# Performance work log

Measured on AMD Instinct MI355X. Metric: run time of the kernel, lower is better.

The kernel has to match this reference:

```python
import jax, jax.numpy as jnp
import numpy as np

B, T, DF, S = 64, 16, 512, 196      # batch, ticks, backbone channels, tokens
D_IN, H = 512, 8                     # attention embed dim, heads
DH = D_IN // H
DM, MEM, HN = 1024, 25, 32           # d_model neurons, memory length, NLM hidden
NSA, NSO, DOUT = 512, 512, 512       # sync sizes (random-pairing), output dim


def _ln(x, g, b, eps=1e-5):
    m = x.mean(-1, keepdims=True)
    v = ((x - m) ** 2).mean(-1, keepdims=True)
    return (x - m) / jnp.sqrt(v + eps) * g + b


def setup_inputs() -> dict:
    key = jax.random.key(0)
    ks = jax.random.split(key, 24)
    rn = lambda k, sh, sc: jax.random.normal(k, sh, jnp.float32) * sc
    p = {}
    p['x'] = rn(ks[0], (B, T, DF, S), 1.0)
    # q_proj (LazyLinear: n_sync_action -> d_input)
    p['Wqp'] = rn(ks[1], (NSA, D_IN), (1.0 / NSA) ** 0.5); p['bqp'] = jnp.zeros((D_IN,))
    # kv_proj: LazyLinear(DF->D_IN) + LayerNorm
    p['Wkv'] = rn(ks[2], (DF, D_IN), (1.0 / DF) ** 0.5); p['bkv'] = jnp.zeros((D_IN,))
    p['g_kv'] = jnp.ones((D_IN,)); p['b_kv'] = jnp.zeros((D_IN,))
    # MultiheadAttention projections
    sc = (1.0 / D_IN) ** 0.5
    p['Wq'] = rn(ks[3], (D_IN, D_IN), sc); p['bq'] = jnp.zeros((D_IN,))
    p['Wk'] = rn(ks[4], (D_IN, D_IN), sc); p['bk'] = jnp.zeros((D_IN,))
    p['Wv'] = rn(ks[5], (D_IN, D_IN), sc); p['bv'] = jnp.zeros((D_IN,))
    p['Wo'] = rn(ks[6], (D_IN, D_IN), sc); p['bo'] = jnp.zeros((D_IN,))
    # synapses: Linear(D_IN+DM -> 2*DM) + GLU + LayerNorm(DM)
    p['Wsyn'] = rn(ks[7], (D_IN + DM, 2 * DM), (1.0 / (D_IN + DM)) ** 0.5)
    p['bsyn'] = jnp.zeros((2 * DM,))
    p['g_syn'] = jnp.ones((DM,)); p['b_syn'] = jnp.zeros((DM,))
    # NLM: per-neuron 2-layer MLP over memory window
    p['W1'] = rn(ks[8], (DM, MEM, HN), (1.0 / MEM) ** 0.5); p['b1'] = jnp.zeros((DM, HN))
    p['W2'] = rn(ks[9], (DM, HN), (1.0 / HN) ** 0.5); p['b2'] = jnp.zeros((DM,))
    # learned initial states
    p['init_act'] = rn(ks[10], (DM,), (1.0 / DM) ** 0.5)
    p['init_hist'] = rn(ks[11], (DM, MEM), (1.0 / (DM + MEM)) ** 0.5)
    # decay params (init zero in torch)
    p['decay_a'] = jnp.zeros((NSA,)); p['decay_o'] = jnp.zeros((NSO,))
    # output projection (LazyLinear: n_sync_out -> d_output)
    p['Wout'] = rn(ks[12], (NSO, DOUT), (1.0 / NSO) ** 0.5); p['bout'] = jnp.zeros((DOUT,))
    # random-pairing neuron indices (buffers, constants)
    p['li_a'] = jax.random.randint(ks[13], (NSA,), 0, DM, jnp.int32)
    p['ri_a'] = jax.random.randint(ks[14], (NSA,), 0, DM, jnp.int32)
    p['li_o'] = jax.random.randint(ks[15], (NSO,), 0, DM, jnp.int32)
    p['ri_o'] = jax.random.randint(ks[16], (NSO,), 0, DM, jnp.int32)
    return p


def reference(x, Wqp, bqp, Wkv, bkv, g_kv, b_kv, Wq, bq, Wk, bk, Wv, bv, Wo, bo,
              Wsyn, bsyn, g_syn, b_syn, W1, b1, W2, b2, init_act, init_hist,
              decay_a, decay_o, Wout, bout, li_a, ri_a, li_o, ri_o):
    r_a = jnp.exp(-jnp.clip(decay_a, 0.0, 15.0))   # [NSA]
    r_o = jnp.exp(-jnp.clip(decay_o, 0.0, 15.0))   # [NSO]
    act0 = jnp.broadcast_to(init_act, (B, DM))
    hist0 = jnp.broadcast_to(init_hist, (B, DM, MEM))
    # initial 'out' sync state (decay_alpha=pairwise, decay_beta=ones)
    ao0 = act0[:, li_o] * act0[:, ri_o]
    bo0 = jnp.ones_like(ao0)
    # 'action' state starts None -> zeros so first update gives alpha=pairwise, beta=1
    aa0 = jnp.zeros((B, NSA), x.dtype); ba0 = jnp.zeros((B, NSA), x.dtype)

    def mha(q, kv):
        # q [B,1,D_IN], kv [B,S,D_IN]
        qh = (q @ Wq + bq).reshape(B, 1, H, DH)
        kh = (kv @ Wk + bk).reshape(B, S, H, DH)
        vh = (kv @ Wv + bv).reshape(B, S, H, DH)
        sc = jnp.einsum('bqhd,bkhd->bhqk', qh, kh) / jnp.sqrt(jnp.float32(DH))
        a = jax.nn.softmax(sc, axis=-1)
        o = jnp.einsum('bhqk,bkhd->bqhd', a, vh).reshape(B, 1, D_IN)
        return o @ Wo + bo

    def tick(carry, xt):
        act, hist, aa, ba, ao, bo_ = carry
        # compute_kv: identity backbone, flatten(2).transpose(1,2) -> [B,S,DF]
        kv = _ln(jnp.swapaxes(xt, 1, 2) @ Wkv + bkv, g_kv, b_kv)
        # action sync
        aa = r_a * aa + act[:, li_a] * act[:, ri_a]
        ba = r_a * ba + 1.0
        sync_a = aa / jnp.sqrt(ba)
        q = (sync_a @ Wqp + bqp)[:, None, :]
        attn = mha(q, kv)[:, 0]                         # [B,D_IN]
        pre = jnp.concatenate([attn, act], axis=-1)     # [B,D_IN+DM]
        g = pre @ Wsyn + bsyn
        a_, b_ = jnp.split(g, 2, axis=-1)
        pre_act = _ln(a_ * jax.nn.sigmoid(b_), g_syn, b_syn)  # [B,DM]
        hist = jnp.concatenate([hist[:, :, 1:], pre_act[:, :, None]], axis=2)
        # NLM: per-neuron MLP over memory window
        h = jax.nn.relu(jnp.einsum('bnm,nmh->bnh', hist, W1) + b1)
        act = jnp.einsum('bnh,nh->bn', h, W2) + b2
        # out sync
        ao = r_o * ao + act[:, li_o] * act[:, ri_o]
        bo_ = r_o * bo_ + 1.0
        sync_o = ao / jnp.sqrt(bo_)
        pred = sync_o @ Wout + bout                      # [B,DOUT]
        logp = jax.nn.log_softmax(pred, axis=-1)
        ne = -(jnp.exp(logp) * logp).sum(-1) / jnp.log(jnp.float32(DOUT))
        cert = jnp.stack([ne, 1.0 - ne], axis=-1)        # [B,2]
        return (act, hist, aa, ba, ao, bo_), (pred, cert)

    xt = jnp.moveaxis(x, 1, 0)  # [T,B,DF,S]
    _, (preds, certs) = jax.lax.scan(tick, (act0, hist0, aa0, ba0, ao0, bo0), xt)
    predictions = jnp.moveaxis(preds, 0, -1)   # [B,DOUT,T]
    certainties = jnp.moveaxis(certs, 0, -1)   # [B,2,T]
    return predictions, certainties
```

## Files before the change

kernel.cpp:

```cpp
#include <hip/hip_runtime.h>
#include <stdint.h>
#include <stddef.h>

#define B_    64
#define T_    16
#define DF_   512
#define S_    196
#define DIN_  512
#define H_    8
#define DH_   64
#define DM_   1024
#define MEM_  25
#define HN_   32
#define MR_   (B_*S_)
#define TC_   2
#define NCH_  (T_/TC_)
#define MCC_  (MR_*TC_)

typedef short bf16x8 __attribute__((ext_vector_type(8)));
typedef short short4v __attribute__((ext_vector_type(4)));
typedef float f32x4  __attribute__((ext_vector_type(4)));

__device__ __forceinline__ float b2f(short h){
  unsigned u = ((unsigned)(unsigned short)h) << 16;
  float f; __builtin_memcpy(&f, &u, 4); return f;
}
__device__ __forceinline__ short f2b(float f){
  unsigned u; __builtin_memcpy(&u, &f, 4);
  u = (u + 0x7fffu + ((u >> 16) & 1u)) >> 16;
  return (short)(unsigned short)u;
}
__device__ __forceinline__ float clip015(float d){
  return d < 0.f ? 0.f : (d > 15.f ? 15.f : d);
}

template<int OUTF32, int LNEPI>
__device__ __forceinline__ void gemm_body(int tid, int bx, int by, int aload,
    short* lA, short* lB,
    const short* __restrict__ A, const short* __restrict__ WT,
    void* __restrict__ Cout,
    const float* __restrict__ biasA, const float* __restrict__ biasB, int nsplit,
    const float* __restrict__ mu, const float* __restrict__ iv,
    const float* __restrict__ gw, const float* __restrict__ bw,
    int M, int N, int K, int lda, int ldc)
{
  const int w = tid >> 6, l = tid & 63;
  const int m0 = bx * 128, n0 = by * 128;
  const int wm = (w >> 1) * 64, wn = (w & 1) * 64;
  f32x4 acc[4][4];
  #pragma unroll
  for (int i=0;i<4;i++)
    #pragma unroll
    for (int j=0;j<4;j++) acc[i][j] = (f32x4){0.f,0.f,0.f,0.f};

  for (int k0 = 0; k0 < K; k0 += 64) {
    #pragma unroll
    for (int rnd = 0; rnd < 4; ++rnd) {
      int cb = (rnd*4 + w) * 64;
      int slot = cb + l;
      int row = slot >> 3, kb = slot & 7;
      int kc = k0 + ((kb ^ (row & 7)) << 3);
      if (aload) {
        int gm = m0 + row; if (gm > M-1) gm = M-1;
        __builtin_amdgcn_global_load_lds(
            (const __attribute__((address_space(1))) void*)(A + (size_t)gm * lda + kc),
            (__attribute__((address_space(3))) void*)&lA[cb*8], 16, 0, 0);
      }
      __builtin_amdgcn_global_load_lds(
          (const __attribute__((address_space(1))) void*)(WT + (size_t)(n0 + row) * K + kc),
          (__attribute__((address_space(3))) void*)&lB[cb*8], 16, 0, 0);
    }
    asm volatile("s_waitcnt vmcnt(0)" ::: "memory");
    __syncthreads();
    #pragma unroll
    for (int ks = 0; ks < 2; ++ks) {
      bf16x8 af[4], bfr[4];
      #pragma unroll
      for (int i = 0; i < 4; ++i) {
        int ra = wm + i*16 + (l & 15);
        int c  = ks*4 + (l >> 4);
        af[i]  = *(const bf16x8*)&lA[ra*64 + ((c ^ (ra & 7)) << 3)];
        int rb = wn + i*16 + (l & 15);
        bfr[i] = *(const bf16x8*)&lB[rb*64 + ((c ^ (rb & 7)) << 3)];
      }
      #pragma unroll
      for (int i = 0; i < 4; ++i)
        #pragma unroll
        for (int j = 0; j < 4; ++j)
          acc[i][j] = __builtin_amdgcn_mfma_f32_16x16x32_bf16(af[i], bfr[j], acc[i][j], 0, 0, 0);
    }
    __syncthreads();
  }
  #pragma unroll
  for (int i = 0; i < 4; ++i) {
    #pragma unroll
    for (int j = 0; j < 4; ++j) {
      int gn = n0 + wn + j*16 + (l & 15);
      float ivn = 0.f, mun = 0.f, bb = 0.f;
      if (LNEPI == 2) { ivn = iv[gn]; mun = mu[gn]; }
      else bb = biasA ? ((gn < nsplit) ? biasA[gn] : biasB[gn - nsplit]) : 0.f;
      #pragma unroll
      for (int r = 0; r < 4; ++r) {
        int gm = m0 + wm + i*16 + (l >> 4)*4 + r;
        if (gm < M) {
          float v;
          if (LNEPI == 2) v = ivn*(acc[i][j][r] - mun*gw[gm]) + bw[gm];
          else            v = acc[i][j][r] + bb;
          if (OUTF32) ((float*)Cout)[(size_t)gm * ldc + gn] = v;
          else        ((short*)Cout)[(size_t)gm * ldc + gn] = f2b(v);
        }
      }
    }
  }
}

template<int OUTF32, int LNEPI>
__global__ __launch_bounds__(256,2) void gemm_k(
    const short* __restrict__ A, const short* __restrict__ WT,
    void* __restrict__ Cout,
    const float* __restrict__ biasA, const float* __restrict__ biasB, int nsplit,
    const float* __restrict__ mu, const float* __restrict__ iv,
    const float* __restrict__ gw, const float* __restrict__ bw,
    int M, int N, int K, int lda, int ldc)
{
  __shared__ short lA[128*64];
  __shared__ short lB[128*64];
  gemm_body<OUTF32,LNEPI>(threadIdx.x, blockIdx.x, blockIdx.y, 1, lA, lB,
                          A, WT, Cout, biasA, biasB, nsplit, mu, iv, gw, bw,
                          M, N, K, lda, ldc);
}

__global__ __launch_bounds__(256,2) void gemm_prep2(
    const short* __restrict__ WqpB, const short* __restrict__ WqT,
    short* __restrict__ WqqB,
    const short* __restrict__ WsynTt, const short* __restrict__ WoB,
    short* __restrict__ WsynF)
{
  __shared__ short lA[128*64];
  __shared__ short lB[128*64];
  int blk = blockIdx.x;
  if (blk < 16)
    gemm_body<0,0>(threadIdx.x, blk & 3, blk >> 2, 1, lA, lB, WqpB, WqT, WqqB,
                   nullptr, nullptr, 1<<30, nullptr, nullptr, nullptr, nullptr,
                   512, 512, 512, 512, 512);
  else {
    int b2 = blk - 16;
    gemm_body<0,0>(threadIdx.x, b2 & 15, b2 >> 4, 1, lA, lB, WsynTt, WoB, WsynF,
                   nullptr, nullptr, 1<<30, nullptr, nullptr, nullptr, nullptr,
                   2048, 512, 512, 512, 1536);
  }
}

__device__ __forceinline__ void run_piggy(int tid, int pb, int pop, int poff,
    char* pool,
    const float* __restrict__ xg, int t0n, short* __restrict__ xT,
    const short* __restrict__ WkvT, const float* __restrict__ bkv,
    short* __restrict__ kvpN, float* __restrict__ muN, float* __restrict__ ivN,
    const short* __restrict__ WkkvT, const float* __restrict__ gw,
    const float* __restrict__ bw, short* __restrict__ KVTN, int McN)
{
  if (pop == 4) {
    int twin = tid >> 8, tid2 = tid & 255;
    float* tile = (float*)(pool + twin*8448);
    int tx = tid2 & 31, ty = tid2 >> 5;
    int base = (poff + pb)*32 + twin*16;
    for (int it = 0; it < 16; ++it) {
      int gt = base + it;
      int df0 = (gt & 15) * 32;
      int r = gt >> 4;
      int s0 = (r % 7) * 32;
      int z = r / 7;
      int b = z >> 1, ti = z & 1;
      const float* src = xg + (size_t)(b*T_ + t0n + ti) * DF_ * S_;
      #pragma unroll
      for (int i = 0; i < 4; ++i) {
        int df = df0 + ty + i*8;
        int s  = s0 + tx;
        tile[(ty+i*8)*33 + tx] = (s < S_) ? src[(size_t)df*S_ + s] : 0.f;
      }
      __syncthreads();
      short* dst = xT + (size_t)((t0n + ti)*B_ + b) * S_ * DIN_;
      #pragma unroll
      for (int i = 0; i < 4; ++i) {
        int s  = s0 + ty + i*8;
        int df = df0 + tx;
        if (s < S_) dst[(size_t)s*DF_ + df] = f2b(tile[tx*33 + ty+i*8]);
      }
      __syncthreads();
    }
  } else if (pop == 1) {
    int twin = tid >> 8;
    short* lA = (short*)pool;
    short* lB = (short*)(pool + 16384 + 16384*twin);
    int p = poff + pb; if (p > 391) p = 391;
    int bx = p % 196, byp = p / 196;
    const short* xTn = xT + (size_t)t0n * MR_ * 512;
    gemm_body<0,0>(tid & 255, bx, byp*2 + twin, twin == 0, lA, lB,
                   xTn, WkvT, kvpN, bkv, bkv, 1 << 30,
                   nullptr, nullptr, nullptr, nullptr,
                   McN, 512, 512, 512, 512);
  } else if (pop == 2) {
    int blk = poff + pb;
    int w = tid >> 6, l = tid & 63;
    for (int i = 0; i < 8; ++i) {
      int r = blk*64 + i*8 + w;
      if (r < McN) {
        bf16x8 v8 = *(const bf16x8*)&kvpN[(size_t)r*512 + l*8];
        float s = 0.f, s2 = 0.f;
        #pragma unroll
        for (int j = 0; j < 8; ++j) { float v = b2f(v8[j]); s += v; s2 += v*v; }
        #pragma unroll
        for (int m = 1; m < 64; m <<= 1) { s += __shfl_xor(s, m, 64); s2 += __shfl_xor(s2, m, 64); }
        if (l == 0) {
          float mean = s * (1.f/512.f);
          float var  = s2 * (1.f/512.f) - mean*mean;
          muN[r] = mean;
          ivN[r] = rsqrtf(var + 1e-5f);
        }
      }
    }
  } else if (pop == 3) {
    int twin = tid >> 8;
    short* lA = (short*)pool;
    short* lB = (short*)(pool + 16384 + 16384*twin);
    int p = poff + pb; if (p > 783) p = 783;
    int bx = p % 8, byp = p / 8;
    gemm_body<0,2>(tid & 255, bx, byp*2 + twin, twin == 0, lA, lB,
                   WkkvT, kvpN, KVTN, nullptr, nullptr, 0,
                   muN, ivN, gw, bw, 1024, McN, 512, 512, McN);
  }
}

__device__ __forceinline__ void attn_body(int b, int tid, float* smem,
    const float* actT, float* aa, float* ba,
    const int* li_a, const int* ri_a, const float* decay_a,
    const short* WqqB, const float* bqh,
    const short* KVT, int ldkv, int ti, short* preb)
{
  float* syncL = smem;
  float* qhL   = smem + 512;
  float* pL    = smem + 1024;
  int j = tid;
  float rr = expf(-clip015(decay_a[j]));
  float prod = actT[li_a[j]*64 + b] * actT[ri_a[j]*64 + b];
  float a2 = rr*aa[b*512+j] + prod; aa[b*512+j] = a2;
  float bb2 = rr*ba[b*512+j] + 1.f;  ba[b*512+j] = bb2;
  syncL[j] = a2 * rsqrtf(bb2);
  __syncthreads();
  float qa = bqh[j];
  #pragma unroll 8
  for (int k = 0; k < 512; ++k) qa += syncL[k]*b2f(WqqB[k*512+j]);
  qhL[j] = qa;
  __syncthreads();
  int h = tid >> 6, l = tid & 63;
  const size_t cb = (size_t)(ti*B_ + b) * S_;
  const short* Kb = KVT + (size_t)(h*64)*ldkv + cb;
  int s3 = 192 + l; int s3c = s3 < S_ ? s3 : S_-1;
  float sc0=0.f, sc1=0.f, sc2=0.f, sc3=0.f;
  #pragma unroll 8
  for (int d = 0; d < 64; ++d) {
    const short* kr = Kb + (size_t)d*ldkv;
    float qv = qhL[h*64 + d];
    sc0 += qv * b2f(kr[l]);
    sc1 += qv * b2f(kr[64 + l]);
    sc2 += qv * b2f(kr[128 + l]);
    sc3 += qv * b2f(kr[s3c]);
  }
  sc0 *= 0.125f; sc1 *= 0.125f; sc2 *= 0.125f;
  sc3 = (s3 < S_) ? sc3*0.125f : -1e30f;
  float mx = fmaxf(fmaxf(sc0, sc1), fmaxf(sc2, sc3));
  #pragma unroll
  for (int k = 32; k >= 1; k >>= 1) mx = fmaxf(mx, __shfl_xor(mx, k, 64));
  float p0 = expf(sc0-mx), p1 = expf(sc1-mx), p2 = expf(sc2-mx), p3 = expf(sc3-mx);
  pL[h*256 + l] = p0; pL[h*256 + 64+l] = p1;
  pL[h*256 + 128+l] = p2; pL[h*256 + 192+l] = p3;
  float ps = p0+p1+p2+p3;
  #pragma unroll
  for (int k = 32; k >= 1; k >>= 1) ps += __shfl_xor(ps, k, 64);
  float inv = 1.f / ps;
  __syncthreads();
  const short4v* vrow = (const short4v*)(KVT + (size_t)(512 + h*64 + l)*ldkv + cb);
  const float* pp = pL + h*256;
  float ac0=0.f, ac1=0.f, ac2=0.f, ac3=0.f;
  #pragma unroll 7
  for (int c = 0; c < 49; ++c) {
    short4v v4 = vrow[c];
    ac0 += pp[c*4]   * b2f(v4.x);
    ac1 += pp[c*4+1] * b2f(v4.y);
    ac2 += pp[c*4+2] * b2f(v4.z);
    ac3 += pp[c*4+3] * b2f(v4.w);
  }
  float accv = (ac0+ac1)+(ac2+ac3);
  preb[(size_t)b*1536 + h*64 + l] = f2b(accv * inv);
}

__device__ __forceinline__ void outk_body(int tt, int b, int tid,
    float* syncL, float* wred,
    const float* actT, float* ao, float* bo_s,
    const int* li_o, const int* ri_o, const float* decay_o,
    const short* WoutB, const float* bout, float* out)
{
  int j = tid;
  float rr = expf(-clip015(decay_o[j]));
  float prod = actT[li_o[j]*64 + b] * actT[ri_o[j]*64 + b];
  float a2 = rr*ao[b*512+j] + prod; ao[b*512+j] = a2;
  float bb2 = rr*bo_s[b*512+j] + 1.f; bo_s[b*512+j] = bb2;
  syncL[j] = a2 * rsqrtf(bb2);
  __syncthreads();
  float a = bout[j];
  #pragma unroll 8
  for (int k = 0; k < 512; ++k) a += syncL[k]*b2f(WoutB[k*512+j]);
  out[((size_t)b*512 + j)*16 + tt] = a;
  int w = tid >> 6, l = tid & 63;
  float m = a;
  #pragma unroll
  for (int k = 32; k >= 1; k >>= 1) m = fmaxf(m, __shfl_xor(m, k, 64));
  if (l == 0) wred[w] = m;
  __syncthreads();
  float M = wred[0];
  #pragma unroll
  for (int k = 1; k < 8; ++k) M = fmaxf(M, wred[k]);
  float e = expf(a - M);
  float z = e, s1 = e*(a - M);
  #pragma unroll
  for (int k = 32; k >= 1; k >>= 1) { z += __shfl_xor(z, k, 64); s1 += __shfl_xor(s1, k, 64); }
  if (l == 0) { wred[8+w] = z; wred[16+w] = s1; }
  __syncthreads();
  if (tid == 0) {
    float Z = 0.f, S1 = 0.f;
    #pragma unroll
    for (int k = 0; k < 8; ++k) { Z += wred[8+k]; S1 += wred[16+k]; }
    float plp = S1 / Z - logf(Z);
    float ne = -plp * (1.f/logf(512.f));
    out[524288 + (size_t)b*32 + tt]      = ne;
    out[524288 + (size_t)b*32 + 16 + tt] = 1.f - ne;
  }
}

__device__ __forceinline__ void synglu_body(int bid, int tid, char* pool,
    const short* preb, const short* WsynP, const float* bsynF, float* u)
{
  f32x4* part = (f32x4*)pool;
  int w = tid >> 6, l = tid & 63;
  int mf = w & 3, kh = w >> 2;
  int arow = mf*16 + (l & 15);
  int kbase = kh*768 + (l >> 4)*8;
  const short* ap = preb + (size_t)arow*1536 + kbase;
  const short* bp = WsynP + (size_t)(bid*16 + (l & 15))*1536 + kbase;
  f32x4 acc = (f32x4){0.f,0.f,0.f,0.f};
  #pragma unroll 4
  for (int ks = 0; ks < 24; ++ks) {
    bf16x8 av = *(const bf16x8*)(ap + ks*32);
    bf16x8 bv = *(const bf16x8*)(bp + ks*32);
    acc = __builtin_amdgcn_mfma_f32_16x16x32_bf16(av, bv, acc, 0, 0, 0);
  }
  part[w*64 + l] = acc;
  __syncthreads();
  if (w < 4) {
    f32x4 o1 = part[w*64 + l], o2 = part[(w+4)*64 + l];
    int c = l & 15;
    int colg = bid*8 + (c & 7);
    float bias = (c < 8) ? bsynF[colg] : bsynF[1024 + colg];
    float tv[4], pv[4];
    #pragma unroll
    for (int r2 = 0; r2 < 4; ++r2) tv[r2] = o1[r2] + o2[r2] + bias;
    #pragma unroll
    for (int r2 = 0; r2 < 4; ++r2) pv[r2] = __shfl_xor(tv[r2], 8, 64);
    if (c < 8) {
      #pragma unroll
      for (int r2 = 0; r2 < 4; ++r2) {
        float uu = tv[r2] * (1.f/(1.f + expf(-pv[r2])));
        int brow = w*16 + (l >> 4)*4 + r2;
        u[brow*1024 + colg] = uu;
      }
    }
  }
}

__device__ __forceinline__ void nlmln_body(int bid, int tid, char* pool,
    const float* u, const float* gsyn, const float* bln, float* hist,
    const float* W1, const float* b1, const float* W2, const float* b2,
    float* actT, short* preb, int t)
{
  float* mstat = (float*)pool;
  float* istat = mstat + 64;
  {
    int b = tid >> 3, p = tid & 7;
    const float* up = u + b*1024 + p*128;
    float s = 0.f, s2 = 0.f;
    #pragma unroll 8
    for (int i = 0; i < 128; ++i) { float v = up[i]; s += v; s2 += v*v; }
    #pragma unroll
    for (int k = 4; k >= 1; k >>= 1) { s += __shfl_xor(s, k, 64); s2 += __shfl_xor(s2, k, 64); }
    if (p == 0) {
      float mean = s * (1.f/1024.f);
      float var  = s2 * (1.f/1024.f) - mean*mean;
      mstat[b] = mean;
      istat[b] = rsqrtf(var + 1e-5f);
    }
  }
  __syncthreads();
  int n = (bid << 3) + (tid >> 6), b = tid & 63;
  float nv = (u[b*1024 + n] - mstat[b]) * istat[b] * gsyn[n] + bln[n];
  int slot = t % MEM_;
  hist[((size_t)n*MEM_ + slot)*64 + b] = nv;
  float h[32];
  #pragma unroll
  for (int j = 0; j < 32; ++j) h[j] = b1[n*32+j];
  #pragma unroll 5
  for (int m = 0; m < MEM_; ++m) {
    int phys = (t + 1 + m) % MEM_;
    float hv = (m == MEM_-1) ? nv : hist[((size_t)n*MEM_ + phys)*64 + b];
    const float* wp = &W1[((size_t)n*MEM_ + m)*32];
    #pragma unroll
    for (int j = 0; j < 32; ++j) h[j] += hv * wp[j];
  }
  float acc = b2[n];
  #pragma unroll
  for (int j = 0; j < 32; ++j) acc += fmaxf(h[j], 0.f) * W2[n*32+j];
  actT[n*64 + b] = acc;
  preb[(size_t)b*1536 + 512 + n] = f2b(acc);
}

#define PIGGY_ARGS int pop, int poff, \
    const float* __restrict__ xg, int t0n, short* __restrict__ xTg, \
    const short* __restrict__ WkvT, \
    const float* __restrict__ bkv, short* __restrict__ kvpN, \
    float* __restrict__ muN, float* __restrict__ ivN, \
    const short* __restrict__ WkkvT, const float* __restrict__ gw, \
    const float* __restrict__ bw, short* __restrict__ KVTN, int McN
#define PIGGY_CALL run_piggy(tid, (int)blockIdx.x - 128, pop, poff, pool, \
    xg, t0n, xTg, WkvT, bkv, kvpN, muN, ivN, WkkvT, gw, bw, KVTN, McN)

__global__ __launch_bounds__(512) void stageA(
    const float* __restrict__ actT,
    float* __restrict__ aa, float* __restrict__ ba,
    const int* __restrict__ li_a, const int* __restrict__ ri_a,
    const float* __restrict__ decay_a,
    const short* __restrict__ WqqB, const float* __restrict__ bqh,
    const short* __restrict__ KVT, int ldkv, int ti,
    short* __restrict__ preb,
    float* __restrict__ ao, float* __restrict__ bo_s,
    const int* __restrict__ li_o, const int* __restrict__ ri_o,
    const float* __restrict__ decay_o,
    const short* __restrict__ WoutB, const float* __restrict__ bout,
    float* __restrict__ out, int t, PIGGY_ARGS)
{
  __shared__ __attribute__((aligned(16))) char pool[49152];
  const int bid = blockIdx.x, tid = threadIdx.x;
  if (bid < 128) {
    float* smem = (float*)pool;
    if (bid < 64)
      attn_body(bid, tid, smem, actT, aa, ba, li_a, ri_a, decay_a,
                WqqB, bqh, KVT, ldkv, ti, preb);
    else if (t > 0)
      outk_body(t-1, bid-64, tid, smem, smem+512, actT, ao, bo_s,
                li_o, ri_o, decay_o, WoutB, bout, out);
  } else {
    PIGGY_CALL;
  }
}

__global__ __launch_bounds__(512) void stageB(
    const short* __restrict__ preb, const short* __restrict__ WsynP,
    const float* __restrict__ bsynF, float* __restrict__ u, PIGGY_ARGS)
{
  __shared__ __attribute__((aligned(16))) char pool[49152];
  const int bid = blockIdx.x, tid = threadIdx.x;
  if (bid < 128) synglu_body(bid, tid, pool, preb, WsynP, bsynF, u);
  else PIGGY_CALL;
}

__global__ __launch_bounds__(512) void stageC(
    const float* __restrict__ u, const float* __restrict__ gsyn,
    const float* __restrict__ bln, float* __restrict__ hist,
    const float* __restrict__ W1, const float* __restrict__ b1,
    const float* __restrict__ W2, const float* __restrict__ b2,
    float* __restrict__ actT, short* __restrict__ preb, int t, PIGGY_ARGS)
{
  __shared__ __attribute__((aligned(16))) char pool[49152];
  const int bid = blockIdx.x, tid = threadIdx.x;
  if (bid < 128) nlmln_body(bid, tid, pool, u, gsyn, bln, hist,
                            W1, b1, W2, b2, actT, preb, t);
  else PIGGY_CALL;
}

__global__ __launch_bounds__(512) void outk_fin(
    const float* __restrict__ actT,
    float* __restrict__ ao, float* __restrict__ bo_s,
    const int* __restrict__ li_o, const int* __restrict__ ri_o,
    const float* __restrict__ decay_o,
    const short* __restrict__ WoutB, const float* __restrict__ bout,
    float* __restrict__ out)
{
  __shared__ __attribute__((aligned(16))) float smem[544];
  outk_body(T_-1, blockIdx.x, threadIdx.x, smem, smem+512, actT, ao, bo_s,
            li_o, ri_o, decay_o, WoutB, bout, out);
}

__global__ __launch_bounds__(256) void xpose_x(const float* __restrict__ x,
                                               short* __restrict__ xT, int t0, int tc)
{
  __shared__ float tile[32][33];
  int df0 = blockIdx.x*32, s0 = blockIdx.y*32;
  int z = blockIdx.z;
  int b = z / tc, ti = z % tc;
  int tx = threadIdx.x & 31, ty = threadIdx.x >> 5;
  const float* src = x + (size_t)(b*T_ + t0 + ti) * DF_ * S_;
  #pragma unroll
  for (int i = 0; i < 4; ++i) {
    int df = df0 + ty + i*8;
    int s  = s0 + tx;
    tile[ty+i*8][tx] = (s < S_) ? src[(size_t)df*S_ + s] : 0.f;
  }
  __syncthreads();
  short* dst = xT + (size_t)((t0 + ti)*B_ + b) * S_ * DIN_;
  #pragma unroll
  for (int i = 0; i < 4; ++i) {
    int s  = s0 + ty + i*8;
    int df = df0 + tx;
    if (s < S_) dst[(size_t)s*DF_ + df] = f2b(tile[tx][ty+i*8]);
  }
}

__global__ __launch_bounds__(256) void ln_stats(const short* __restrict__ in,
    float* __restrict__ mu, float* __restrict__ iv, int nrows)
{
  int w = threadIdx.x >> 6, l = threadIdx.x & 63;
  int r = blockIdx.x*4 + w;
  if (r >= nrows) return;
  bf16x8 v8 = *(const bf16x8*)&in[(size_t)r*512 + l*8];
  float s = 0.f, s2 = 0.f;
  #pragma unroll
  for (int j = 0; j < 8; ++j) { float v = b2f(v8[j]); s += v; s2 += v*v; }
  #pragma unroll
  for (int m = 1; m < 64; m <<= 1) { s += __shfl_xor(s, m, 64); s2 += __shfl_xor(s2, m, 64); }
  if (l == 0) {
    float mean = s * (1.f/512.f);
    float var  = s2 * (1.f/512.f) - mean*mean;
    mu[r] = mean;
    iv[r] = rsqrtf(var + 1e-5f);
  }
}

__global__ __launch_bounds__(256) void permrows(const short* __restrict__ in,
                                                short* __restrict__ out)
{
  int r = blockIdx.x;
  int k = r >> 4, i = r & 15;
  int src = (i < 8) ? (k*8 + i) : (1024 + k*8 + (i - 8));
  const bf16x8* s = (const bf16x8*)(in + (size_t)src*1536);
  bf16x8* d = (bf16x8*)(out + (size_t)r*1536);
  int j = threadIdx.x;
  if (j < 192) d[j] = s[j];
}

__global__ __launch_bounds__(256) void prep_all(
    const float* __restrict__ Wkv, const float* __restrict__ Wk,
    const float* __restrict__ Wv,  const float* __restrict__ Wsyn,
    const float* __restrict__ Wq,  const float* __restrict__ Wqp,
    const float* __restrict__ Wo,  const float* __restrict__ Wout,
    const float* __restrict__ g_kv, const float* __restrict__ b_kv,
    const float* __restrict__ bk, const float* __restrict__ bv,
    const float* __restrict__ bqp, const float* __restrict__ bq,
    const float* __restrict__ bo_p, const float* __restrict__ bsyn,
    short* __restrict__ WkvT, short* __restrict__ WkkvT,
    short* __restrict__ WsynF, short* __restrict__ WsynTt,
    short* __restrict__ WqT, short* __restrict__ WqpB,
    short* __restrict__ WoB, short* __restrict__ WoutB,
    float* __restrict__ bqh, float* __restrict__ bsynF,
    float* __restrict__ gw, float* __restrict__ bw,
    float* __restrict__ aa, float* __restrict__ ba,
    float* __restrict__ ao, float* __restrict__ bo_s,
    float* __restrict__ actT, float* __restrict__ hist,
    short* __restrict__ preb,
    const float* __restrict__ init_act, const float* __restrict__ init_hist,
    const int* __restrict__ li_o, const int* __restrict__ ri_o)
{
  __shared__ float tile[32][33];
  const int blk = blockIdx.x, tid = threadIdx.x;
  auto wtr = [&](const float* in, short* out, int bx, int by,
                 int C, int ldo, int coff, const float* scale){
    int c0 = bx*32, r0 = by*32;
    int tx = tid & 31, ty = tid >> 5;
    #pragma unroll
    for (int i = 0; i < 4; ++i) {
      int r = r0+ty+i*8;
      float sc = scale ? scale[r] : 1.f;
      tile[ty+i*8][tx] = in[(size_t)r*C + c0+tx] * sc;
    }
    __syncthreads();
    #pragma unroll
    for (int i = 0; i < 4; ++i)
      out[(size_t)(c0+ty+i*8)*ldo + coff + r0+tx] = f2b(tile[tx][ty+i*8]);
  };
  auto cvt4 = [&](const float* in, short* out, int sb){
    int i = (sb*256 + tid)*4;
    #pragma unroll
    for (int j = 0; j < 4; ++j) out[i+j] = f2b(in[i+j]);
  };
  auto bfold = [&](const float* vec, const float* W, const float* base,
                   float* out, int n, int ldw){
    float a = base ? base[n] : 0.f;
    #pragma unroll 8
    for (int k = 0; k < 512; ++k) a += vec[k]*W[(size_t)k*ldw + n];
    out[n] = a;
  };

  if (blk < 256)       wtr(Wkv, WkvT, blk & 15, blk >> 4, 512, 512, 0, nullptr);
  else if (blk < 512)  { int s = blk-256;  wtr(Wk, WkkvT, s & 15, s >> 4, 512, 512, 0, g_kv); }
  else if (blk < 768)  { int s = blk-512;  wtr(Wv, WkkvT + (size_t)512*512, s & 15, s >> 4, 512, 512, 0, g_kv); }
  else if (blk < 2816) { int s = blk-768;  wtr(Wsyn + (size_t)512*2048, WsynF, s % 64, s / 64, 2048, 1536, 512, nullptr); }
  else if (blk < 3840) { int s = blk-2816; wtr(Wsyn, WsynTt, s % 64, s / 64, 2048, 512, 0, nullptr); }
  else if (blk < 4096) { int s = blk-3840; wtr(Wq, WqT, s & 15, s >> 4, 512, 512, 0, nullptr); }
  else if (blk < 4352) cvt4(Wqp,  WqpB,  blk-4096);
  else if (blk < 4608) cvt4(Wo,   WoB,   blk-4352);
  else if (blk < 4864) cvt4(Wout, WoutB, blk-4608);
  else if (blk < 4882) {
    int j = blk-4864;
    if (j < 2)        bfold(bqp,  Wq,   bq,   bqh,   j*256 + tid,      512);
    else if (j < 10)  bfold(bo_p, Wsyn, bsyn, bsynF, (j-2)*256 + tid,  2048);
    else if (j < 12)  bfold(g_kv, Wk,   nullptr, gw,       (j-10)*256 + tid, 512);
    else if (j < 14)  bfold(g_kv, Wv,   nullptr, gw + 512, (j-12)*256 + tid, 512);
    else if (j < 16)  bfold(b_kv, Wk,   bk,   bw,       (j-14)*256 + tid, 512);
    else              bfold(b_kv, Wv,   bv,   bw + 512, (j-16)*256 + tid, 512);
  } else {
    int i = (blk-4882)*256 + tid;
    if (i < 64*512) {
      aa[i] = 0.f; ba[i] = 0.f;
      int j = i & 511;
      ao[i] = init_act[li_o[j]] * init_act[ri_o[j]];
      bo_s[i] = 1.f;
    }
    if (i < 65536) {
      int n = i >> 6, b = i & 63;
      actT[i] = init_act[n];
      preb[(size_t)b*1536 + 512 + n] = f2b(init_act[n]);
    }
    if (i < DM_*MEM_*64) {
      int nm = i >> 6;
      hist[i] = init_hist[nm];
    }
  }
}

extern "C" void kernel_launch(void* const* d_in, const int* in_sizes, int n_in,
                              void* d_out, int out_size, void* d_ws, size_t ws_size,
                              hipStream_t stream)
{
  (void)in_sizes; (void)n_in; (void)out_size;
  const float* x       = (const float*)d_in[0];
  const float* Wqp     = (const float*)d_in[1];
  const float* bqp     = (const float*)d_in[2];
  const float* Wkv     = (const float*)d_in[3];
  const float* bkv     = (const float*)d_in[4];
  const float* g_kv    = (const float*)d_in[5];
  const float* b_kv    = (const float*)d_in[6];
  const float* Wq      = (const float*)d_in[7];
  const float* bq      = (const float*)d_in[8];
  const float* Wk      = (const float*)d_in[9];
  const float* bk      = (const float*)d_in[10];
  const float* Wv      = (const float*)d_in[11];
  const float* bv      = (const float*)d_in[12];
  const float* Wo      = (const float*)d_in[13];
  const float* bo_p    = (const float*)d_in[14];
  const float* Wsyn    = (const float*)d_in[15];
  const float* bsyn    = (const float*)d_in[16];
  const float* g_syn   = (const float*)d_in[17];
  const float* b_syn   = (const float*)d_in[18];
  const float* W1      = (const float*)d_in[19];
  const float* b1      = (const float*)d_in[20];
  const float* W2      = (const float*)d_in[21];
  const float* b2      = (const float*)d_in[22];
  const float* init_act  = (const float*)d_in[23];
  const float* init_hist = (const float*)d_in[24];
  const float* decay_a = (const float*)d_in[25];
  const float* decay_o = (const float*)d_in[26];
  const float* Wout    = (const float*)d_in[27];
  const float* bout    = (const float*)d_in[28];
  const int* li_a = (const int*)d_in[29];
  const int* ri_a = (const int*)d_in[30];
  const int* li_o = (const int*)d_in[31];
  const int* ri_o = (const int*)d_in[32];

  char* ws = (char*)d_ws;
  size_t off = 0;
  auto alloc = [&](size_t bytes) { char* p = ws + off; off += (bytes + 255) & ~(size_t)255; return p; };
  short* WkvT   = (short*)alloc(512*512*2);
  short* WkkvT  = (short*)alloc(1024*512*2);
  short* WsynF  = (short*)alloc(2048*1536*2);
  short* WsynP  = (short*)alloc(2048*1536*2);
  short* WsynTt = (short*)alloc(2048*512*2);
  short* WqpB   = (short*)alloc(512*512*2);
  short* WqT    = (short*)alloc(512*512*2);
  short* WoB    = (short*)alloc(512*512*2);
  short* WqqB   = (short*)alloc(512*512*2);
  short* WoutB  = (short*)alloc(512*512*2);
  float* bqh    = (float*)alloc(512*4);
  float* bsynF  = (float*)alloc(2048*4);
  float* gw     = (float*)alloc(1024*4);
  float* bw     = (float*)alloc(1024*4);
  short* preb   = (short*)alloc(64*1536*2);
  float* u      = (float*)alloc(64*1024*4);
  float* aa     = (float*)alloc(64*512*4);
  float* ba     = (float*)alloc(64*512*4);
  float* ao     = (float*)alloc(64*512*4);
  float* bo_s   = (float*)alloc(64*512*4);
  float* actT   = (float*)alloc(1024*64*4);
  float* hist   = (float*)alloc((size_t)1024*25*64*4);
  size_t fixed_end = off;

  const size_t szXT  = (size_t)T_*MR_*512*2;
  const size_t szKVP = (size_t)MCC_*512*2;
  const size_t szKVT = (size_t)MCC_*1024*2;
  const size_t szST  = (size_t)MCC_*4;
  size_t need_full = fixed_end + szXT + 2*szKVP + 2*szKVT + 4*szST + 4096;
  bool pig_en = (ws_size >= need_full);

  short* xT = (short*)alloc(szXT);
  short* kvpB[2]; short* KVTB[2]; float* muB[2]; float* ivB[2];
  kvpB[0] = (short*)alloc(szKVP);
  KVTB[0] = (short*)alloc(szKVT);
  muB[0]  = (float*)alloc(szST);
  ivB[0]  = (float*)alloc(szST);
  if (pig_en) {
    kvpB[1] = (short*)alloc(szKVP);
    KVTB[1] = (short*)alloc(szKVT);
    muB[1]  = (float*)alloc(szST);
    ivB[1]  = (float*)alloc(szST);
  } else {
    kvpB[1] = kvpB[0]; KVTB[1] = KVTB[0]; muB[1] = muB[0]; ivB[1] = ivB[0];
  }

  const int BIG = 1 << 30;
  const float* FN = nullptr;

  prep_all<<<11282, 256, 0, stream>>>(Wkv, Wk, Wv, Wsyn, Wq, Wqp, Wo, Wout,
      g_kv, b_kv, bk, bv, bqp, bq, bo_p, bsyn,
      WkvT, WkkvT, WsynF, WsynTt, WqT, WqpB, WoB, WoutB,
      bqh, bsynF, gw, bw, aa, ba, ao, bo_s, actT, hist, preb,
      init_act, init_hist, li_o, ri_o);
  gemm_prep2<<<80, 256, 0, stream>>>(WqpB, WqT, WqqB, WsynTt, WoB, WsynF);
  permrows<<<2048, 256, 0, stream>>>(WsynF, WsynP);

  if (pig_en)
    xpose_x<<<dim3(16,7,B_*TC_), 256, 0, stream>>>(x, xT, 0, TC_);
  else
    xpose_x<<<dim3(16,7,B_*T_), 256, 0, stream>>>(x, xT, 0, T_);

  auto run_pipe = [&](int c, short* kvpP, float* muP, float* ivP, short* KVTP){
    const short* xTc = xT + (size_t)c*TC_*MR_*512;
    gemm_k<0,0><<<dim3(196,4), 256, 0, stream>>>(xTc, WkvT, kvpP, bkv, bkv, BIG,
                                                 FN, FN, FN, FN, MCC_, 512, 512, 512, 512);
    ln_stats<<<MCC_/4, 256, 0, stream>>>(kvpP, muP, ivP, MCC_);
    gemm_k<0,2><<<dim3(8,196), 256, 0, stream>>>(WkkvT, kvpP, KVTP, nullptr, nullptr, BIG,
                                                 muP, ivP, gw, bw, 1024, MCC_, 512, 512, MCC_);
  };

  auto pigcfg = [](int q, bool pig, int& op, int& pf, int& n){
    op = 0; pf = 0; n = 0;
    if (!pig) return;
    if (q == 0)      { op = 4; pf = 0;         n = 448; }
    else if (q == 1) { op = 1; pf = 0;         n = 392; }
    else if (q == 2) { op = 2; pf = 0;         n = 392; }
    else             { op = 3; pf = (q-3)*262; n = (q == 5) ? 260 : 262; }
  };

  run_pipe(0, kvpB[0], muB[0], ivB[0], KVTB[0]);

  for (int c = 0; c < NCH_; ++c) {
    int par = pig_en ? (c & 1) : 0;
    int nxt = pig_en ? (par ^ 1) : 0;
    if (!pig_en && c > 0) run_pipe(c, kvpB[0], muB[0], ivB[0], KVTB[0]);
    bool pig = pig_en && (c < NCH_-1);
    int t0n = (c < NCH_-1) ? (c+1)*TC_ : 0;
    for (int ti = 0; ti < TC_; ++ti) {
      int t = c*TC_ + ti;
      int op, pf, n;
      pigcfg(ti*3+0, pig, op, pf, n);
      stageA<<<128+n, 512, 0, stream>>>(actT, aa, ba, li_a, ri_a, decay_a,
          WqqB, bqh, KVTB[par], MCC_, ti, preb,
          ao, bo_s, li_o, ri_o, decay_o, WoutB, bout, (float*)d_out, t,
          op, pf, x, t0n, xT, WkvT, bkv, kvpB[nxt], muB[nxt], ivB[nxt],
          WkkvT, gw, bw, KVTB[nxt], MCC_);
      pigcfg(ti*3+1, pig, op, pf, n);
      stageB<<<128+n, 512, 0, stream>>>(preb, WsynP, bsynF, u,
          op, pf, x, t0n, xT, WkvT, bkv, kvpB[nxt], muB[nxt], ivB[nxt],
          WkkvT, gw, bw, KVTB[nxt], MCC_);
      pigcfg(ti*3+2, pig, op, pf, n);
      stageC<<<128+n, 512, 0, stream>>>(u, g_syn, b_syn, hist,
          W1, b1, W2, b2, actT, preb, t,
          op, pf, x, t0n, xT, WkvT, bkv, kvpB[nxt], muB[nxt], ivB[nxt],
          WkkvT, gw, bw, KVTB[nxt], MCC_);
    }
  }
  outk_fin<<<64, 512, 0, stream>>>(actT, ao, bo_s, li_o, ri_o, decay_o,
                                   WoutB, bout, (float*)d_out);
}
```

Baseline: 2.027 ms.

## Deepen piggyback pipeline: transpose two chunks ahead and fuse prologue kernels

The transpose of x is now piggybacked two chunks ahead, split across the first two stages alongside the KV projection GEMM of the next chunk. Each stage launch can therefore run two piggyback ops. The prologue is also fused: prep_all transposes the first two chunks, gemm_prep3 runs the chunk-0 KV GEMM next to the weight GEMMs, and permstats merges the row permutation with the LN stats. The goal is to cut serialized startup launches and spread background work more evenly across ticks, at the cost of more complex block-index dispatch and heavier stage launches.

```diff
diff --git a/kernel.cpp b/kernel.cpp
--- a/kernel.cpp
+++ b/kernel.cpp
@@ -130,11 +130,13 @@
                           M, N, K, lda, ldc);
 }
 
-__global__ __launch_bounds__(256,2) void gemm_prep2(
+__global__ __launch_bounds__(256,2) void gemm_prep3(
     const short* __restrict__ WqpB, const short* __restrict__ WqT,
     short* __restrict__ WqqB,
     const short* __restrict__ WsynTt, const short* __restrict__ WoB,
-    short* __restrict__ WsynF)
+    short* __restrict__ WsynF,
+    const short* __restrict__ xT, const short* __restrict__ WkvT,
+    const float* __restrict__ bkv, short* __restrict__ kvp0)
 {
   __shared__ short lA[128*64];
   __shared__ short lB[128*64];
@@ -143,27 +145,64 @@
     gemm_body<0,0>(threadIdx.x, blk & 3, blk >> 2, 1, lA, lB, WqpB, WqT, WqqB,
                    nullptr, nullptr, 1<<30, nullptr, nullptr, nullptr, nullptr,
                    512, 512, 512, 512, 512);
-  else {
+  else if (blk < 80) {
     int b2 = blk - 16;
     gemm_body<0,0>(threadIdx.x, b2 & 15, b2 >> 4, 1, lA, lB, WsynTt, WoB, WsynF,
                    nullptr, nullptr, 1<<30, nullptr, nullptr, nullptr, nullptr,
                    2048, 512, 512, 512, 1536);
-  }
-}
-
-__device__ __forceinline__ void run_piggy(int tid, int pb, int pop, int poff,
+  } else {
+    int p = blk - 80;
+    gemm_body<0,0>(threadIdx.x, p % 196, p / 196, 1, lA, lB, xT, WkvT, kvp0,
+                   bkv, bkv, 1<<30, nullptr, nullptr, nullptr, nullptr,
+                   MCC_, 512, 512, 512, 512);
+  }
+}
+
+__global__ __launch_bounds__(256) void permstats(
+    const short* __restrict__ WsynF, short* __restrict__ WsynP,
+    const short* __restrict__ kvp0, float* __restrict__ mu0,
+    float* __restrict__ iv0)
+{
+  int blk = blockIdx.x, tid = threadIdx.x;
+  if (blk < 2048) {
+    int r = blk;
+    int k = r >> 4, i = r & 15;
+    int src = (i < 8) ? (k*8 + i) : (1024 + k*8 + (i - 8));
+    const bf16x8* s = (const bf16x8*)(WsynF + (size_t)src*1536);
+    bf16x8* d = (bf16x8*)(WsynP + (size_t)r*1536);
+    if (tid < 192) d[tid] = s[tid];
+  } else {
+    int w = tid >> 6, l = tid & 63;
+    int r = (blk-2048)*4 + w;
+    if (r >= MCC_) return;
+    bf16x8 v8 = *(const bf16x8*)&kvp0[(size_t)r*512 + l*8];
+    float s = 0.f, s2 = 0.f;
+    #pragma unroll
+    for (int j = 0; j < 8; ++j) { float v = b2f(v8[j]); s += v; s2 += v*v; }
+    #pragma unroll
+    for (int m = 1; m < 64; m <<= 1) { s += __shfl_xor(s, m, 64); s2 += __shfl_xor(s2, m, 64); }
+    if (l == 0) {
+      float mean = s * (1.f/512.f);
+      float var  = s2 * (1.f/512.f) - mean*mean;
+      mu0[r] = mean;
+      iv0[r] = rsqrtf(var + 1e-5f);
+    }
+  }
+}
+
+__device__ __forceinline__ void run_piggy(int tid, int op, int idx,
     char* pool,
-    const float* __restrict__ xg, int t0n, short* __restrict__ xT,
+    const float* __restrict__ xg, int t0n1, int t0n2, short* __restrict__ xT,
     const short* __restrict__ WkvT, const float* __restrict__ bkv,
     short* __restrict__ kvpN, float* __restrict__ muN, float* __restrict__ ivN,
     const short* __restrict__ WkkvT, const float* __restrict__ gw,
     const float* __restrict__ bw, short* __restrict__ KVTN, int McN)
 {
-  if (pop == 4) {
+  if (op == 4) {
     int twin = tid >> 8, tid2 = tid & 255;
     float* tile = (float*)(pool + twin*8448);
     int tx = tid2 & 31, ty = tid2 >> 5;
-    int base = (poff + pb)*32 + twin*16;
+    int base = idx*32 + twin*16;
     for (int it = 0; it < 16; ++it) {
       int gt = base + it;
       int df0 = (gt & 15) * 32;
@@ -171,7 +210,7 @@
       int s0 = (r % 7) * 32;
       int z = r / 7;
       int b = z >> 1, ti = z & 1;
-      const float* src = xg + (size_t)(b*T_ + t0n + ti) * DF_ * S_;
+      const float* src = xg + (size_t)(b*T_ + t0n2 + ti) * DF_ * S_;
       #pragma unroll
       for (int i = 0; i < 4; ++i) {
         int df = df0 + ty + i*8;
@@ -179,7 +218,7 @@
         tile[(ty+i*8)*33 + tx] = (s < S_) ? src[(size_t)df*S_ + s] : 0.f;
       }
       __syncthreads();
-      short* dst = xT + (size_t)((t0n + ti)*B_ + b) * S_ * DIN_;
+      short* dst = xT + (size_t)((t0n2 + ti)*B_ + b) * S_ * DIN_;
       #pragma unroll
       for (int i = 0; i < 4; ++i) {
         int s  = s0 + ty + i*8;
@@ -188,19 +227,19 @@
       }
       __syncthreads();
     }
-  } else if (pop == 1) {
+  } else if (op == 1) {
     int twin = tid >> 8;
     short* lA = (short*)pool;
     short* lB = (short*)(pool + 16384 + 16384*twin);
-    int p = poff + pb; if (p > 391) p = 391;
+    int p = idx; if (p > 391) p = 391;
     int bx = p % 196, byp = p / 196;
-    const short* xTn = xT + (size_t)t0n * MR_ * 512;
+    const short* xTn = xT + (size_t)t0n1 * MR_ * 512;
     gemm_body<0,0>(tid & 255, bx, byp*2 + twin, twin == 0, lA, lB,
                    xTn, WkvT, kvpN, bkv, bkv, 1 << 30,
                    nullptr, nullptr, nullptr, nullptr,
                    McN, 512, 512, 512, 512);
-  } else if (pop == 2) {
-    int blk = poff + pb;
+  } else if (op == 2) {
+    int blk = idx;
     int w = tid >> 6, l = tid & 63;
     for (int i = 0; i < 8; ++i) {
       int r = blk*64 + i*8 + w;
@@ -219,11 +258,11 @@
         }
       }
     }
-  } else if (pop == 3) {
+  } else if (op == 3) {
     int twin = tid >> 8;
     short* lA = (short*)pool;
     short* lB = (short*)(pool + 16384 + 16384*twin);
-    int p = poff + pb; if (p > 783) p = 783;
+    int p = idx; if (p > 783) p = 783;
     int bx = p % 8, byp = p / 8;
     gemm_body<0,2>(tid & 255, bx, byp*2 + twin, twin == 0, lA, lB,
                    WkkvT, kvpN, KVTN, nullptr, nullptr, 0,
@@ -422,15 +461,21 @@
   preb[(size_t)b*1536 + 512 + n] = f2b(acc);
 }
 
-#define PIGGY_ARGS int pop, int poff, \
-    const float* __restrict__ xg, int t0n, short* __restrict__ xTg, \
+#define PIGGY_ARGS int opA, int pfA, int nA, int opB, int pfB, \
+    const float* __restrict__ xg, int t0n1, int t0n2, short* __restrict__ xTg, \
     const short* __restrict__ WkvT, \
     const float* __restrict__ bkv, short* __restrict__ kvpN, \
     float* __restrict__ muN, float* __restrict__ ivN, \
     const short* __restrict__ WkkvT, const float* __restrict__ gw, \
     const float* __restrict__ bw, short* __restrict__ KVTN, int McN
-#define PIGGY_CALL run_piggy(tid, (int)blockIdx.x - 128, pop, poff, pool, \
-    xg, t0n, xTg, WkvT, bkv, kvpN, muN, ivN, WkkvT, gw, bw, KVTN, McN)
+#define PIGGY_CALL do { \
+    int pb = (int)blockIdx.x - 128; \
+    int op_, idx_; \
+    if (pb < nA) { op_ = opA; idx_ = pfA + pb; } \
+    else         { op_ = opB; idx_ = pfB + (pb - nA); } \
+    run_piggy(tid, op_, idx_, pool, xg, t0n1, t0n2, xTg, WkvT, bkv, \
+              kvpN, muN, ivN, WkkvT, gw, bw, KVTN, McN); \
+  } while (0)
 
 __global__ __launch_bounds__(512) void stageA(
     const float* __restrict__ actT,
@@ -541,18 +586,6 @@
     mu[r] = mean;
     iv[r] = rsqrtf(var + 1e-5f);
   }
-}
-
-__global__ __launch_bounds__(256) void permrows(const short* __restrict__ in,
-                                                short* __restrict__ out)
-{
-  int r = blockIdx.x;
-  int k = r >> 4, i = r & 15;
-  int src = (i < 8) ? (k*8 + i) : (1024 + k*8 + (i - 8));
-  const bf16x8* s = (const bf16x8*)(in + (size_t)src*1536);
-  bf16x8* d = (bf16x8*)(out + (size_t)r*1536);
-  int j = threadIdx.x;
-  if (j < 192) d[j] = s[j];
 }
 
 __global__ __launch_bounds__(256) void prep_all(
@@ -575,7 +608,8 @@
     float* __restrict__ actT, float* __restrict__ hist,
     short* __restrict__ preb,
     const float* __restrict__ init_act, const float* __restrict__ init_hist,
-    const int* __restrict__ li_o, const int* __restrict__ ri_o)
+    const int* __restrict__ li_o, const int* __restrict__ ri_o,
+    const float* __restrict__ x, short* __restrict__ xT)
 {
   __shared__ float tile[32][33];
   const int blk = blockIdx.x, tid = threadIdx.x;
@@ -624,7 +658,7 @@
     else if (j < 14)  bfold(g_kv, Wv,   nullptr, gw + 512, (j-12)*256 + tid, 512);
     else if (j < 16)  bfold(b_kv, Wk,   bk,   bw,       (j-14)*256 + tid, 512);
     else              bfold(b_kv, Wv,   bv,   bw + 512, (j-16)*256 + tid, 512);
-  } else {
+  } else if (blk < 11282) {
     int i = (blk-4882)*256 + tid;
     if (i < 64*512) {
       aa[i] = 0.f; ba[i] = 0.f;
@@ -640,6 +674,33 @@
     if (i < DM_*MEM_*64) {
       int nm = i >> 6;
       hist[i] = init_hist[nm];
+    }
+  } else {
+    int tx = tid & 31, ty = tid >> 5;
+    int base = (blk - 11282) * 16;
+    for (int it = 0; it < 16; ++it) {
+      int gt = base + it;
+      int df0 = (gt & 15) * 32;
+      int r = gt >> 4;
+      int s0 = (r % 7) * 32;
+      int z = r / 7;
+      int b = z >> 2, t = z & 3;
+      const float* src = x + (size_t)(b*T_ + t) * DF_ * S_;
+      #pragma unroll
+      for (int i = 0; i < 4; ++i) {
+        int df = df0 + ty + i*8;
+        int s  = s0 + tx;
+        tile[ty+i*8][tx] = (s < S_) ? src[(size_t)df*S_ + s] : 0.f;
+      }
+      __syncthreads();
+      short* dst = xT + (size_t)(t*B_ + b) * S_ * DIN_;
+      #pragma unroll
+      for (int i = 0; i < 4; ++i) {
+        int s  = s0 + ty + i*8;
+        int df = df0 + tx;
+        if (s < S_) dst[(size_t)s*DF_ + df] = f2b(tile[tx][ty+i*8]);
+      }
+      __syncthreads();
     }
   }
 }
@@ -735,18 +796,18 @@
   const int BIG = 1 << 30;
   const float* FN = nullptr;
 
-  prep_all<<<11282, 256, 0, stream>>>(Wkv, Wk, Wv, Wsyn, Wq, Wqp, Wo, Wout,
+  prep_all<<<13074, 256, 0, stream>>>(Wkv, Wk, Wv, Wsyn, Wq, Wqp, Wo, Wout,
       g_kv, b_kv, bk, bv, bqp, bq, bo_p, bsyn,
       WkvT, WkkvT, WsynF, WsynTt, WqT, WqpB, WoB, WoutB,
       bqh, bsynF, gw, bw, aa, ba, ao, bo_s, actT, hist, preb,
-      init_act, init_hist, li_o, ri_o);
-  gemm_prep2<<<80, 256, 0, stream>>>(WqpB, WqT, WqqB, WsynTt, WoB, WsynF);
-  permrows<<<2048, 256, 0, stream>>>(WsynF, WsynP);
-
-  if (pig_en)
-    xpose_x<<<dim3(16,7,B_*TC_), 256, 0, stream>>>(x, xT, 0, TC_);
-  else
-    xpose_x<<<dim3(16,7,B_*T_), 256, 0, stream>>>(x, xT, 0, T_);
+      init_act, init_hist, li_o, ri_o, x, xT);
+  if (!pig_en)
+    xpose_x<<<dim3(16,7,B_*(T_-2*TC_)), 256, 0, stream>>>(x, xT, 2*TC_, T_-2*TC_);
+  gemm_prep3<<<864, 256, 0, stream>>>(WqpB, WqT, WqqB, WsynTt, WoB, WsynF,
+                                      xT, WkvT, bkv, kvpB[0]);
+  permstats<<<2048 + MCC_/4, 256, 0, stream>>>(WsynF, WsynP, kvpB[0], muB[0], ivB[0]);
+  gemm_k<0,2><<<dim3(8,196), 256, 0, stream>>>(WkkvT, kvpB[0], KVTB[0], nullptr, nullptr, BIG,
+                                               muB[0], ivB[0], gw, bw, 1024, MCC_, 512, 512, MCC_);
 
   auto run_pipe = [&](int c, short* kvpP, float* muP, float* ivP, short* KVTP){
     const short* xTc = xT + (size_t)c*TC_*MR_*512;
@@ -757,41 +818,45 @@
                                                  muP, ivP, gw, bw, 1024, MCC_, 512, 512, MCC_);
   };
 
-  auto pigcfg = [](int q, bool pig, int& op, int& pf, int& n){
-    op = 0; pf = 0; n = 0;
-    if (!pig) return;
-    if (q == 0)      { op = 4; pf = 0;         n = 448; }
-    else if (q == 1) { op = 1; pf = 0;         n = 392; }
-    else if (q == 2) { op = 2; pf = 0;         n = 392; }
-    else             { op = 3; pf = (q-3)*262; n = (q == 5) ? 260 : 262; }
+  auto pigcfg = [](int q, bool p123, bool p4,
+                   int& opA, int& pfA, int& nA, int& opB, int& pfB, int& nB){
+    opA = 0; pfA = 0; nA = 0; opB = 0; pfB = 0; nB = 0;
+    if (q == 0 || q == 1) {
+      if (p123) { opA = 1; pfA = q*196; nA = 196; }
+      if (p4)   { opB = 4; pfB = q*224; nB = 224; }
+    } else if (q == 2) {
+      if (p123) { opA = 2; pfA = 0; nA = 392; }
+    } else {
+      if (p123) { opA = 3; pfA = (q-3)*262; nA = (q == 5) ? 260 : 262; }
+    }
   };
-
-  run_pipe(0, kvpB[0], muB[0], ivB[0], KVTB[0]);
 
   for (int c = 0; c < NCH_; ++c) {
     int par = pig_en ? (c & 1) : 0;
     int nxt = pig_en ? (par ^ 1) : 0;
     if (!pig_en && c > 0) run_pipe(c, kvpB[0], muB[0], ivB[0], KVTB[0]);
-    bool pig = pig_en && (c < NCH_-1);
-    int t0n = (c < NCH_-1) ? (c+1)*TC_ : 0;
+    bool p123 = pig_en && (c < NCH_-1);
+    bool p4   = pig_en && (c < NCH_-2);
+    int t0n1 = (c < NCH_-1) ? (c+1)*TC_ : 0;
+    int t0n2 = (c < NCH_-2) ? (c+2)*TC_ : 0;
     for (int ti = 0; ti < TC_; ++ti) {
       int t = c*TC_ + ti;
-      int op, pf, n;
-      pigcfg(ti*3+0, pig, op, pf, n);
-      stageA<<<128+n, 512, 0, stream>>>(actT, aa, ba, li_a, ri_a, decay_a,
+      int oA, fA, nA, oB, fB, nB;
+      pigcfg(ti*3+0, p123, p4, oA, fA, nA, oB, fB, nB);
+      stageA<<<128+nA+nB, 512, 0, stream>>>(actT, aa, ba, li_a, ri_a, decay_a,
           WqqB, bqh, KVTB[par], MCC_, ti, preb,
           ao, bo_s, li_o, ri_o, decay_o, WoutB, bout, (float*)d_out, t,
-          op, pf, x, t0n, xT, WkvT, bkv, kvpB[nxt], muB[nxt], ivB[nxt],
-          WkkvT, gw, bw, KVTB[nxt], MCC_);
-      pigcfg(ti*3+1, pig, op, pf, n);
-      stageB<<<128+n, 512, 0, stream>>>(preb, WsynP, bsynF, u,
-          op, pf, x, t0n, xT, WkvT, bkv, kvpB[nxt], muB[nxt], ivB[nxt],
-          WkkvT, gw, bw, KVTB[nxt], MCC_);
-      pigcfg(ti*3+2, pig, op, pf, n);
-      stageC<<<128+n, 512, 0, stream>>>(u, g_syn, b_syn, hist,
+          oA, fA, nA, oB, fB, x, t0n1, t0n2, xT, WkvT, bkv,
+          kvpB[nxt], muB[nxt], ivB[nxt], WkkvT, gw, bw, KVTB[nxt], MCC_);
+      pigcfg(ti*3+1, p123, p4, oA, fA, nA, oB, fB, nB);
+      stageB<<<128+nA+nB, 512, 0, stream>>>(preb, WsynP, bsynF, u,
+          oA, fA, nA, oB, fB, x, t0n1, t0n2, xT, WkvT, bkv,
+          kvpB[nxt], muB[nxt], ivB[nxt], WkkvT, gw, bw, KVTB[nxt], MCC_);
+      pigcfg(ti*3+2, p123, p4, oA, fA, nA, oB, fB, nB);
+      stageC<<<128+nA+nB, 512, 0, stream>>>(u, g_syn, b_syn, hist,
           W1, b1, W2, b2, actT, preb, t,
-          op, pf, x, t0n, xT, WkvT, bkv, kvpB[nxt], muB[nxt], ivB[nxt],
-          WkkvT, gw, bw, KVTB[nxt], MCC_);
+          oA, fA, nA, oB, fB, x, t0n1, t0n2, xT, WkvT, bkv,
+          kvpB[nxt], muB[nxt], ivB[nxt], WkkvT, gw, bw, KVTB[nxt], MCC_);
     }
   }
   outk_fin<<<64, 512, 0, stream>>>(actT, ao, bo_s, li_o, ri_o, decay_o,
```

After: 2.046 ms (median of 2 runs). About the same (+0.9%).
